# Optimization experiments

Measured on AMD Instinct MI355X. Metric: run time of the kernel, lower is better.

Reference implementation:

```python
import jax, jax.numpy as jnp
import numpy as np

N, E, C, ED = 50000, 800000, 128, 16
NEG_SLOPE = 0.2


def setup_inputs() -> dict:
    key = jax.random.key(0)
    ks = jax.random.split(key, 18)
    inp = {
        "h": jax.random.normal(ks[0], (N, C), jnp.float32),
        "edge_index": jax.random.randint(ks[1], (2, E), 0, N),
        "edge_attr": jax.random.normal(ks[2], (E, ED), jnp.float32),
        "reducible": jax.random.randint(ks[3], (N,), 0, 2) > 0,
    }
    names = ["W", "att_src", "att_dst", "W_edge", "att_edge", "W_res", "bias"]
    shapes = [(C, C), (C,), (C,), (ED, C), (C,), (C, C), (C,)]
    i = 4
    for pre in ["red_", "irr_"]:
        for n, sh in zip(names, shapes):
            inp[pre + n] = jax.random.normal(ks[i], sh, jnp.float32) * 0.05
            i += 1
    return inp


def _gat_conv(h, src, dst, edge_attr, W, att_src, att_dst, W_edge, att_edge, W_res, bias):
    """PyG GATConv (heads=1, residual=True, add_self_loops=True, fill_value='mean')."""
    n = h.shape[0]
    # self-loop edge_attr = mean of incoming edge_attr per node (0 if none)
    sum_attr = jax.ops.segment_sum(edge_attr, dst, num_segments=n)
    cnt = jax.ops.segment_sum(jnp.ones((edge_attr.shape[0],), edge_attr.dtype), dst, num_segments=n)
    mean_attr = sum_attr / jnp.maximum(cnt, 1.0)[:, None]
    loop = jnp.arange(n)
    s = jnp.concatenate([src, loop])   # [E+N]
    d = jnp.concatenate([dst, loop])   # [E+N]
    ea = jnp.concatenate([edge_attr, mean_attr], axis=0)  # [E+N, ED]
    x = h @ W                              # [N, C]
    a_src = x @ att_src                    # [N]
    a_dst = x @ att_dst                    # [N]
    a_edge = (ea @ W_edge) @ att_edge      # [E+N]
    alpha = jax.nn.leaky_relu(a_src[s] + a_dst[d] + a_edge, NEG_SLOPE)
    # per-destination softmax (every node has a self-loop -> denom > 0)
    m = jax.ops.segment_max(alpha, d, num_segments=n)
    ex = jnp.exp(alpha - m[d])
    denom = jax.ops.segment_sum(ex, d, num_segments=n)
    w = ex / denom[d]                      # [E+N]
    out = jax.ops.segment_sum(w[:, None] * x[s], d, num_segments=n)  # [N, C]
    return out + h @ W_res + bias


def reference(h, edge_index, edge_attr, reducible,
              red_W, red_att_src, red_att_dst, red_W_edge, red_att_edge, red_W_res, red_bias,
              irr_W, irr_att_src, irr_att_dst, irr_W_edge, irr_att_edge, irr_W_res, irr_bias):
    src, dst = edge_index[0], edge_index[1]
    out_r = _gat_conv(h, src, dst, edge_attr, red_W, red_att_src, red_att_dst,
                      red_W_edge, red_att_edge, red_W_res, red_bias)
    out_i = _gat_conv(h, src, dst, edge_attr, irr_W, irr_att_src, irr_att_dst,
                      irr_W_edge, irr_att_edge, irr_W_res, irr_bias)
    return jax.nn.relu(jnp.where(reducible[:, None], out_r, out_i))
```

## Files before the change

### kernel.cpp

```cpp
#include <hip/hip_runtime.h>
#include <hip/hip_bf16.h>

#define CDIM 128
#define EDIM 16
#define NEG_SLOPE 0.2f

typedef __attribute__((ext_vector_type(8))) short bf16x8;
typedef __attribute__((ext_vector_type(4))) float f32x4;
typedef __attribute__((ext_vector_type(2))) float f32x2;
typedef unsigned int uint;
typedef unsigned short ushort;

__device__ __forceinline__ ushort f2bf(float f) {
    uint u = __float_as_uint(f);
    return (ushort)((u + 0x7fffu + ((u >> 16) & 1u)) >> 16);
}
__device__ __forceinline__ uint packbf(float lo, float hi) {
    return ((uint)f2bf(hi) << 16) | (uint)f2bf(lo);
}
__device__ __forceinline__ float bflo(uint w) { return __uint_as_float(w << 16); }
__device__ __forceinline__ float bfhi(uint w) { return __uint_as_float(w & 0xffff0000u); }

__device__ __forceinline__ bool redtest(const void* red, int i, int notInt, int notFloat) {
    if (!notInt)        return ((const int*)red)[i] != 0;
    else if (!notFloat) return ((const float*)red)[i] != 0.f;
    else                return ((const unsigned char*)red)[i] != 0;
}

__global__ void bcatwe_kernel(const float* __restrict__ Wr, const float* __restrict__ Wi,
                              const float* __restrict__ Wrr, const float* __restrict__ Wri,
                              ushort* __restrict__ BT,
                              const float* __restrict__ WeR, const float* __restrict__ aeR,
                              const float* __restrict__ WeI, const float* __restrict__ aeI,
                              float* __restrict__ we) {
    if (blockIdx.x < 256) {
        int idx = blockIdx.x * 256 + threadIdx.x;
        int c = idx >> 7, k = idx & 127;
        const float* srcm;
        if (c < 128)      srcm = Wr;
        else if (c < 256) srcm = Wi;
        else if (c < 384) srcm = Wrr;
        else              srcm = Wri;
        BT[idx] = f2bf(srcm[k * 128 + (c & 127)]);
    } else {
        int lane = threadIdx.x;
        if (lane < 16) {
            float s = 0.f;
            for (int c = 0; c < CDIM; ++c) s += WeR[lane * CDIM + c] * aeR[c];
            we[lane] = s;
        } else if (lane < 32) {
            int j = lane - 16;
            float s = 0.f;
            for (int c = 0; c < CDIM; ++c) s += WeI[j * CDIM + c] * aeI[c];
            we[16 + j] = s;
        }
    }
}

__global__ __launch_bounds__(256) void prep_kernel(const uint* __restrict__ red, int nwords,
                                                   int* __restrict__ flags,
                                                   const int* __restrict__ dst, int* __restrict__ cnt,
                                                   int* __restrict__ rank,
                                                   const float* __restrict__ ea, const float* __restrict__ we,
                                                   uint* __restrict__ escal4, int E) {
    int i = blockIdx.x * 256 + threadIdx.x;
    if (i < nwords) {
        uint w = red[i];
        bool isInt = (w <= 1u);
        bool isFloat = (w == 0u) || (w == 0x3f800000u);
        if (!isInt) atomicOr(&flags[0], 1);
        if (!isFloat) atomicOr(&flags[1], 1);
    }
    if (i < E) {
        int r = atomicAdd(&cnt[dst[i]], 1);
        __builtin_nontemporal_store(r, rank + i);
        const f32x4* row = (const f32x4*)(ea + (size_t)i * EDIM);
        const float4* we4 = (const float4*)we;
        float er = 0.f, ei = 0.f;
#pragma unroll
        for (int q = 0; q < 4; ++q) {
            f32x4 v = __builtin_nontemporal_load(row + q);
            float4 wr = we4[q], wi = we4[4 + q];
            er += v.x * wr.x + v.y * wr.y + v.z * wr.z + v.w * wr.w;
            ei += v.x * wi.x + v.y * wi.y + v.z * wi.z + v.w * wi.w;
        }
        __builtin_nontemporal_store(packbf(er, ei), escal4 + i);
    }
}

__global__ __launch_bounds__(256) void gemm_dots(const float* __restrict__ h,
                                                 const ushort* __restrict__ BT,
                                                 ushort* __restrict__ C,
                                                 const float* __restrict__ attsr, const float* __restrict__ attdr,
                                                 const float* __restrict__ attsi, const float* __restrict__ attdi,
                                                 float* __restrict__ asr, float* __restrict__ adr,
                                                 float* __restrict__ asi, float* __restrict__ adi, int M) {
    __shared__ ushort As[128 * 128];
    __shared__ ushort Bs[128 * 128];
    __shared__ float dots[2][128];
    int t = threadIdx.x;
    int lane = t & 63, wv = t >> 6;
    int rb = blockIdx.x * 128, cb = blockIdx.y * 128;
    int by = blockIdx.y;

    if (t < 128) { dots[0][t] = 0.f; dots[1][t] = 0.f; }

    int rsub = wv * 4 + (lane >> 4);
    int c0 = lane & 15;
#pragma unroll
    for (int p = 0; p < 8; ++p) {
        int row = p * 16 + rsub;
        int chunk = c0 ^ (row & 7);
        const ushort* gb = BT + (size_t)(cb + row) * 128 + chunk * 8;
        __builtin_amdgcn_global_load_lds(
            (const __attribute__((address_space(1))) void*)gb,
            (__attribute__((address_space(3))) void*)((char*)Bs + p * 4096 + wv * 1024),
            16, 0, 0);
    }

    {
        int row = t >> 1, half = t & 1;
        int gra = rb + row; if (gra > M - 1) gra = M - 1;
        const float4* hp = (const float4*)(h + (size_t)gra * 128 + half * 64);
#pragma unroll
        for (int k = 0; k < 8; ++k) {
            float4 a = hp[2 * k], b = hp[2 * k + 1];
            uint4 o;
            o.x = packbf(a.x, a.y); o.y = packbf(a.z, a.w);
            o.z = packbf(b.x, b.y); o.w = packbf(b.z, b.w);
            int c = half * 8 + k;
            *(uint4*)((char*)As + row * 256 + (c ^ (row & 7)) * 16) = o;
        }
    }
    __syncthreads();

    int wr = wv >> 1, wc = wv & 1;
    int l15 = lane & 15, l4 = lane >> 4;
    f32x4 acc[4][4];
#pragma unroll
    for (int i = 0; i < 4; ++i)
#pragma unroll
        for (int j = 0; j < 4; ++j) acc[i][j] = (f32x4){0.f, 0.f, 0.f, 0.f};

    const char* Ab = (const char*)As;
    const char* Bb = (const char*)Bs;
#pragma unroll
    for (int ks = 0; ks < 4; ++ks) {
        bf16x8 a[4], b[4];
#pragma unroll
        for (int f = 0; f < 4; ++f) {
            int row = wr * 64 + f * 16 + l15;
            int ch = (ks * 4 + l4) ^ (row & 7);
            a[f] = *(const bf16x8*)(Ab + row * 256 + ch * 16);
            int col = wc * 64 + f * 16 + l15;
            int ch2 = (ks * 4 + l4) ^ (col & 7);
            b[f] = *(const bf16x8*)(Bb + col * 256 + ch2 * 16);
        }
#pragma unroll
        for (int i = 0; i < 4; ++i)
#pragma unroll
            for (int j = 0; j < 4; ++j)
                acc[i][j] = __builtin_amdgcn_mfma_f32_16x16x32_bf16(a[i], b[j], acc[i][j], 0, 0, 0);
    }

    if (by < 2) {
        const float* attS = by ? attsi : attsr;
        const float* attD = by ? attdi : attdr;
        float aS[4], aD[4];
#pragma unroll
        for (int j = 0; j < 4; ++j) {
            int c = wc * 64 + j * 16 + l15;
            aS[j] = attS[c]; aD[j] = attD[c];
        }
#pragma unroll
        for (int i = 0; i < 4; ++i)
#pragma unroll
            for (int rr = 0; rr < 4; ++rr) {
                float ps = 0.f, pd = 0.f;
#pragma unroll
                for (int j = 0; j < 4; ++j) {
                    float v = acc[i][j][rr];
                    ps += v * aS[j]; pd += v * aD[j];
                }
#pragma unroll
                for (int d = 1; d < 16; d <<= 1) {
                    ps += __shfl_xor(ps, d); pd += __shfl_xor(pd, d);
                }
                if (l15 == 0) {
                    int row = wr * 64 + i * 16 + l4 * 4 + rr;
                    atomicAdd(&dots[0][row], ps);
                    atomicAdd(&dots[1][row], pd);
                }
            }
    }

#pragma unroll
    for (int i = 0; i < 4; ++i) {
        int rl = wr * 64 + i * 16 + l4 * 4;
#pragma unroll
        for (int j = 0; j < 4; ++j) {
            int col = cb + wc * 64 + j * 16 + l15;
#pragma unroll
            for (int r = 0; r < 4; ++r) {
                int gr = rb + rl + r;
                if (gr < M) C[(size_t)gr * 512 + col] = f2bf(acc[i][j][r]);
            }
        }
    }

    if (by < 2) {
        __syncthreads();
        if (t < 128) {
            int gr = rb + t;
            if (gr < M) {
                if (by == 0) { asr[gr] = dots[0][t]; adr[gr] = dots[1][t]; }
                else         { asi[gr] = dots[0][t]; adi[gr] = dots[1][t]; }
            }
        }
    }
}

__global__ __launch_bounds__(256) void scanA_kernel(const int* __restrict__ cnt,
                                                    int* __restrict__ offA,
                                                    int* __restrict__ bsum, int n) {
    __shared__ int wsum[4];
    int t = threadIdx.x, lane = t & 63, wid = t >> 6;
    int i0 = blockIdx.x * 1024 + t * 4;
    int v[4];
#pragma unroll
    for (int j = 0; j < 4; ++j) { int i = i0 + j; v[j] = (i < n) ? cnt[i] : 0; }
    int s = v[0] + v[1] + v[2] + v[3];
    int incl = s;
#pragma unroll
    for (int d = 1; d < 64; d <<= 1) { int u = __shfl_up(incl, d); if (lane >= d) incl += u; }
    if (lane == 63) wsum[wid] = incl;
    __syncthreads();
    int wpre = 0;
    for (int w = 0; w < wid; ++w) wpre += wsum[w];
    int run = wpre + incl - s;
#pragma unroll
    for (int j = 0; j < 4; ++j) {
        int i = i0 + j;
        if (i < n) offA[i] = run;
        run += v[j];
    }
    if (t == 255) bsum[blockIdx.x] = wpre + incl;
}

__global__ void scanB_kernel(int* __restrict__ bsum, int nb) {
    int lane = threadIdx.x;
    int carry = 0;
    for (int base = 0; base < nb; base += 64) {
        int i = base + lane;
        int v = (i < nb) ? bsum[i] : 0;
        int incl = v;
#pragma unroll
        for (int d = 1; d < 64; d <<= 1) { int u = __shfl_up(incl, d); if (lane >= d) incl += u; }
        if (i < nb) bsum[i] = carry + incl - v;
        carry += __shfl(incl, 63);
    }
}

__global__ __launch_bounds__(256) void scatter_kernel(
    const int* __restrict__ src, const int* __restrict__ dst,
    const int* __restrict__ rank, const uint* __restrict__ escal4,
    const void* __restrict__ red, const int* __restrict__ flags,
    const int* __restrict__ offA, const int* __restrict__ bsum,
    uint* __restrict__ csr, int E) {
    int e = blockIdx.x * 256 + threadIdx.x;
    if (e >= E) return;
    int s = __builtin_nontemporal_load(src + e);
    int d = __builtin_nontemporal_load(dst + e);
    uint ee = __builtin_nontemporal_load(escal4 + e);
    int rk = __builtin_nontemporal_load(rank + e);
    int notInt = flags[0], notFloat = flags[1];
    bool rr = redtest(red, d, notInt, notFloat);
    uint evb = rr ? (ee & 0xffffu) : (ee >> 16);
    int off = offA[d] + bsum[d >> 10];
    csr[off + rk] = (uint)s | (evb << 16);
}

__global__ __launch_bounds__(256) void node_kernel(
    const ushort* __restrict__ xcat,
    const float* __restrict__ adst_r, const float* __restrict__ adst_i,
    const float* __restrict__ asrc_r, const float* __restrict__ asrc_i,
    const void* __restrict__ red, const int* __restrict__ flags,
    const int* __restrict__ offA, const int* __restrict__ bsum,
    const uint* __restrict__ csr,
    const float* __restrict__ bias_r, const float* __restrict__ bias_i,
    float* __restrict__ out, int n, int E) {
    __shared__ uint2 buf[4][64];
    int wv = threadIdx.x >> 6, lane = threadIdx.x & 63;
    int node = blockIdx.x * 4 + wv;
    if (node >= n) return;

    int notInt = flags[0], notFloat = flags[1];
    bool r = redtest(red, node, notInt, notFloat);

    const float* asrc = r ? asrc_r : asrc_i;
    float adst = (r ? adst_r : adst_i)[node];
    uint vsel = r ? 0u : 256u;
    int b0 = offA[node] + bsum[node >> 10];
    int b1 = (node + 1 < n) ? (offA[node + 1] + bsum[(node + 1) >> 10]) : E;
    int k = b1 - b0;
    const char* xb = (const char*)xcat;
    uint lane4 = lane * 4;

    float m = -1e30f, denom = 0.f;
    float2 acca = make_float2(0.f, 0.f), accb = make_float2(0.f, 0.f);
    float sumE = 0.f;

    for (int base = b0; base < b1; base += 64) {
        int j = base + lane;
        float al = -1e30f; uint soff = 0;
        if (j < b1) {
            uint rec = __builtin_nontemporal_load(csr + j);
            uint s = rec & 0xffffu;
            float ev = bfhi(rec);
            sumE += ev;
            soff = s * 1024u + vsel;
            float a = asrc[s] + ev + adst;
            al = (a >= 0.f) ? a : NEG_SLOPE * a;
        }
        float cm = al;
#pragma unroll
        for (int d = 32; d; d >>= 1) cm = fmaxf(cm, __shfl_xor(cm, d));
        float mn = fmaxf(m, cm);
        float sc = __expf(m - mn);
        denom *= sc;
        acca.x *= sc; acca.y *= sc; accb.x *= sc; accb.y *= sc;
        m = mn;
        float ex = (j < b1) ? __expf(al - mn) : 0.f;
        buf[wv][lane] = make_uint2(__float_as_uint(ex), soff);
        __builtin_amdgcn_wave_barrier();
        int cc = min(64, b1 - base);
        int ccp = (cc + 7) & ~7;
        for (int tq = 0; tq < ccp; tq += 8) {
            uint2 u[8];
#pragma unroll
            for (int q = 0; q < 8; ++q) u[q] = buf[wv][tq + q];
            uint v[8];
#pragma unroll
            for (int q = 0; q < 8; ++q) v[q] = *(const uint*)(xb + u[q].y + lane4);
#pragma unroll
            for (int q = 0; q < 4; ++q) {
                float w = __uint_as_float(u[q].x);
                acca.x += w * bflo(v[q]); acca.y += w * bfhi(v[q]);
            }
#pragma unroll
            for (int q = 4; q < 8; ++q) {
                float w = __uint_as_float(u[q].x);
                accb.x += w * bflo(v[q]); accb.y += w * bfhi(v[q]);
            }
        }
        float exs = ex;
#pragma unroll
        for (int d = 32; d; d >>= 1) exs += __shfl_xor(exs, d);
        denom += exs;
        __builtin_amdgcn_wave_barrier();
    }
    float acc0 = acca.x + accb.x, acc1 = acca.y + accb.y;

#pragma unroll
    for (int d = 32; d; d >>= 1) sumE += __shfl_xor(sumE, d);
    float eself = sumE / fmaxf((float)k, 1.f);
    float a = asrc[node] + adst + eself;
    float aself = (a >= 0.f) ? a : NEG_SLOPE * a;
    float mn = fmaxf(m, aself);
    float sc = __expf(m - mn);
    float exl = __expf(aself - mn);
    denom = denom * sc + exl;
    uint voff = (uint)node * 1024u + vsel;
    uint vsw = *(const uint*)(xb + voff + lane4);
    acc0 = acc0 * sc + exl * bflo(vsw);
    acc1 = acc1 * sc + exl * bfhi(vsw);

    float inv = 1.f / denom;
    uint roff = (uint)node * 1024u + (r ? 512u : 768u);
    uint bw = *(const uint*)(xb + roff + lane4);
    float2 bi2 = ((const float2*)(r ? bias_r : bias_i))[lane];
    f32x2 o;
    o.x = fmaxf(acc0 * inv + bflo(bw) + bi2.x, 0.f);
    o.y = fmaxf(acc1 * inv + bfhi(bw) + bi2.y, 0.f);
    __builtin_nontemporal_store(o, ((f32x2*)out) + (size_t)node * 64 + lane);
}

extern "C" void kernel_launch(void* const* d_in, const int* in_sizes, int n_in,
                              void* d_out, int out_size, void* d_ws, size_t ws_size,
                              hipStream_t stream) {
    const float* h          = (const float*)d_in[0];
    const int*   edge_index = (const int*)d_in[1];
    const float* edge_attr  = (const float*)d_in[2];
    const void*  reducible  = d_in[3];
    const float* red_W      = (const float*)d_in[4];
    const float* red_att_src= (const float*)d_in[5];
    const float* red_att_dst= (const float*)d_in[6];
    const float* red_W_edge = (const float*)d_in[7];
    const float* red_att_edge=(const float*)d_in[8];
    const float* red_W_res  = (const float*)d_in[9];
    const float* red_bias   = (const float*)d_in[10];
    const float* irr_W      = (const float*)d_in[11];
    const float* irr_att_src= (const float*)d_in[12];
    const float* irr_att_dst= (const float*)d_in[13];
    const float* irr_W_edge = (const float*)d_in[14];
    const float* irr_att_edge=(const float*)d_in[15];
    const float* irr_W_res  = (const float*)d_in[16];
    const float* irr_bias   = (const float*)d_in[17];

    const int N = in_sizes[0] / CDIM;
    const int E = in_sizes[1] / 2;
    const int* src = edge_index;
    const int* dst = edge_index + E;
    const int nb = (N + 1023) / 1024;

    float* out = (float*)d_out;

    size_t cur = 0;
    auto alloc = [&](size_t bytes) { size_t p = cur; cur = (cur + bytes + 255) & ~(size_t)255; return p; };
    char* ws = (char*)d_ws;
    size_t o_xcat  = alloc((size_t)N * 512 * 2);
    size_t o_bcat  = alloc(512 * 128 * 2);
    size_t o_we    = alloc(256);
    size_t o_asr   = alloc((size_t)N * 4);
    size_t o_adr   = alloc((size_t)N * 4);
    size_t o_asi   = alloc((size_t)N * 4);
    size_t o_adi   = alloc((size_t)N * 4);
    size_t o_flags = alloc(256);
    size_t o_cnt   = alloc((size_t)N * 4);
    size_t o_offA  = alloc((size_t)N * 4);
    size_t o_bsum  = alloc((size_t)(nb + 1) * 4);
    size_t o_rank  = alloc((size_t)E * 4);
    size_t o_escal = alloc((size_t)E * 4);
    size_t o_csr   = alloc((size_t)E * 4);
    if (cur > ws_size) return;

    ushort* xcat = (ushort*)(ws + o_xcat);
    ushort* bcat = (ushort*)(ws + o_bcat);
    float* we    = (float*)(ws + o_we);
    float* asr   = (float*)(ws + o_asr);
    float* adr   = (float*)(ws + o_adr);
    float* asi   = (float*)(ws + o_asi);
    float* adi   = (float*)(ws + o_adi);
    int*   flags = (int*)(ws + o_flags);
    int*   cnt   = (int*)(ws + o_cnt);
    int*   offA  = (int*)(ws + o_offA);
    int*   bsum  = (int*)(ws + o_bsum);
    int*   rank  = (int*)(ws + o_rank);
    uint*  escal4= (uint*)(ws + o_escal);
    uint*  csr   = (uint*)(ws + o_csr);

    hipMemsetAsync(flags, 0, 8, stream);
    hipMemsetAsync(cnt, 0, (size_t)N * 4, stream);

    bcatwe_kernel<<<257, 256, 0, stream>>>(red_W, irr_W, red_W_res, irr_W_res, bcat,
                                           red_W_edge, red_att_edge, irr_W_edge, irr_att_edge, we);

    int nwords = N / 4;
    prep_kernel<<<(E + 255) / 256, 256, 0, stream>>>((const uint*)reducible, nwords, flags,
                                                     dst, cnt, rank, edge_attr, we, escal4, E);

    dim3 ggrid((N + 127) / 128, 4);
    gemm_dots<<<ggrid, 256, 0, stream>>>(h, bcat, xcat,
                                         red_att_src, red_att_dst,
                                         irr_att_src, irr_att_dst,
                                         asr, adr, asi, adi, N);

    scanA_kernel<<<nb, 256, 0, stream>>>(cnt, offA, bsum, N);
    scanB_kernel<<<1, 64, 0, stream>>>(bsum, nb);

    scatter_kernel<<<(E + 255) / 256, 256, 0, stream>>>(src, dst, rank, escal4,
                                                        reducible, flags, offA, bsum, csr, E);

    node_kernel<<<(N + 3) / 4, 256, 0, stream>>>(xcat, adr, adi, asr, asi,
                                                 reducible, flags, offA, bsum, csr,
                                                 red_bias, irr_bias, out, N, E);
}
```

Before: 169.2 us.

## Pre-convert h to bf16 in prep kernel and skip unneeded residual GEMM stores

```diff
diff --git a/kernel.cpp b/kernel.cpp
--- a/kernel.cpp
+++ b/kernel.cpp
@@ -62,7 +62,9 @@
                                                    const int* __restrict__ dst, int* __restrict__ cnt,
                                                    int* __restrict__ rank,
                                                    const float* __restrict__ ea, const float* __restrict__ we,
-                                                   uint* __restrict__ escal4, int E) {
+                                                   uint* __restrict__ escal4,
+                                                   const float* __restrict__ h, ushort* __restrict__ hbf,
+                                                   int E, int n4) {
     int i = blockIdx.x * 256 + threadIdx.x;
     if (i < nwords) {
         uint w = red[i];
@@ -86,24 +88,39 @@
         }
         __builtin_nontemporal_store(packbf(er, ei), escal4 + i);
     }
-}
-
-__global__ __launch_bounds__(256) void gemm_dots(const float* __restrict__ h,
+    if (i < n4) {
+        f32x4 v = __builtin_nontemporal_load((const f32x4*)h + i);
+        uint2 o;
+        o.x = packbf(v.x, v.y);
+        o.y = packbf(v.z, v.w);
+        ((uint2*)hbf)[i] = o;
+    }
+}
+
+__global__ __launch_bounds__(256) void gemm_dots(const ushort* __restrict__ A,
                                                  const ushort* __restrict__ BT,
                                                  ushort* __restrict__ C,
                                                  const float* __restrict__ attsr, const float* __restrict__ attdr,
                                                  const float* __restrict__ attsi, const float* __restrict__ attdi,
                                                  float* __restrict__ asr, float* __restrict__ adr,
-                                                 float* __restrict__ asi, float* __restrict__ adi, int M) {
+                                                 float* __restrict__ asi, float* __restrict__ adi,
+                                                 const void* __restrict__ red, const int* __restrict__ flags,
+                                                 int M) {
     __shared__ ushort As[128 * 128];
     __shared__ ushort Bs[128 * 128];
     __shared__ float dots[2][128];
+    __shared__ unsigned char redrow[128];
     int t = threadIdx.x;
     int lane = t & 63, wv = t >> 6;
     int rb = blockIdx.x * 128, cb = blockIdx.y * 128;
     int by = blockIdx.y;
 
     if (t < 128) { dots[0][t] = 0.f; dots[1][t] = 0.f; }
+    if (by >= 2 && t < 128) {
+        int gr = rb + t;
+        int notInt = flags[0], notFloat = flags[1];
+        redrow[t] = (gr < M) ? (redtest(red, gr, notInt, notFloat) ? 1 : 0) : 0;
+    }
 
     int rsub = wv * 4 + (lane >> 4);
     int c0 = lane & 15;
@@ -111,26 +128,17 @@
     for (int p = 0; p < 8; ++p) {
         int row = p * 16 + rsub;
         int chunk = c0 ^ (row & 7);
+        int gra = rb + row; if (gra > M - 1) gra = M - 1;
+        const ushort* ga = A + (size_t)gra * 128 + chunk * 8;
+        __builtin_amdgcn_global_load_lds(
+            (const __attribute__((address_space(1))) void*)ga,
+            (__attribute__((address_space(3))) void*)((char*)As + p * 4096 + wv * 1024),
+            16, 0, 0);
         const ushort* gb = BT + (size_t)(cb + row) * 128 + chunk * 8;
         __builtin_amdgcn_global_load_lds(
             (const __attribute__((address_space(1))) void*)gb,
             (__attribute__((address_space(3))) void*)((char*)Bs + p * 4096 + wv * 1024),
             16, 0, 0);
-    }
-
-    {
-        int row = t >> 1, half = t & 1;
-        int gra = rb + row; if (gra > M - 1) gra = M - 1;
-        const float4* hp = (const float4*)(h + (size_t)gra * 128 + half * 64);
-#pragma unroll
-        for (int k = 0; k < 8; ++k) {
-            float4 a = hp[2 * k], b = hp[2 * k + 1];
-            uint4 o;
-            o.x = packbf(a.x, a.y); o.y = packbf(a.z, a.w);
-            o.z = packbf(b.x, b.y); o.w = packbf(b.z, b.w);
-            int c = half * 8 + k;
-            *(uint4*)((char*)As + row * 256 + (c ^ (row & 7)) * 16) = o;
-        }
     }
     __syncthreads();
 
@@ -203,7 +211,10 @@
 #pragma unroll
             for (int r = 0; r < 4; ++r) {
                 int gr = rb + rl + r;
-                if (gr < M) C[(size_t)gr * 512 + col] = f2bf(acc[i][j][r]);
+                bool doit = gr < M;
+                if (by == 2) doit = doit && redrow[rl + r];
+                else if (by == 3) doit = doit && !redrow[rl + r];
+                if (doit) C[(size_t)gr * 512 + col] = f2bf(acc[i][j][r]);
             }
         }
     }
@@ -412,6 +423,7 @@
     const int* src = edge_index;
     const int* dst = edge_index + E;
     const int nb = (N + 1023) / 1024;
+    const int n4 = N * 128 / 4;
 
     float* out = (float*)d_out;
 
@@ -419,6 +431,7 @@
     auto alloc = [&](size_t bytes) { size_t p = cur; cur = (cur + bytes + 255) & ~(size_t)255; return p; };
     char* ws = (char*)d_ws;
     size_t o_xcat  = alloc((size_t)N * 512 * 2);
+    size_t o_hbf   = alloc((size_t)N * 128 * 2);
     size_t o_bcat  = alloc(512 * 128 * 2);
     size_t o_we    = alloc(256);
     size_t o_asr   = alloc((size_t)N * 4);
@@ -435,6 +448,7 @@
     if (cur > ws_size) return;
 
     ushort* xcat = (ushort*)(ws + o_xcat);
+    ushort* hbf  = (ushort*)(ws + o_hbf);
     ushort* bcat = (ushort*)(ws + o_bcat);
     float* we    = (float*)(ws + o_we);
     float* asr   = (float*)(ws + o_asr);
@@ -456,14 +470,17 @@
                                            red_W_edge, red_att_edge, irr_W_edge, irr_att_edge, we);
 
     int nwords = N / 4;
-    prep_kernel<<<(E + 255) / 256, 256, 0, stream>>>((const uint*)reducible, nwords, flags,
-                                                     dst, cnt, rank, edge_attr, we, escal4, E);
+    int pgrid = (max(E, n4) + 255) / 256;
+    prep_kernel<<<pgrid, 256, 0, stream>>>((const uint*)reducible, nwords, flags,
+                                           dst, cnt, rank, edge_attr, we, escal4,
+                                           h, hbf, E, n4);
 
     dim3 ggrid((N + 127) / 128, 4);
-    gemm_dots<<<ggrid, 256, 0, stream>>>(h, bcat, xcat,
+    gemm_dots<<<ggrid, 256, 0, stream>>>(hbf, bcat, xcat,
                                          red_att_src, red_att_dst,
                                          irr_att_src, irr_att_dst,
-                                         asr, adr, asi, adi, N);
+                                         asr, adr, asi, adi,
+                                         reducible, flags, N);
 
     scanA_kernel<<<nb, 256, 0, stream>>>(cnt, offA, bsum, N);
     scanB_kernel<<<1, 64, 0, stream>>>(bsum, nb);
```

Measured after the change: 170.8 us. No clear change (+0.9%).
